# Performance work log

Hardware: AMD Instinct MI355X
Metric: run time of the kernel (lower is better)

## Reference

```python
import jax, jax.numpy as jnp
import numpy as np

ND, NT, B = 16384, 16384, 4096
FD, FT, C = 256, 256, 768


def _gat(x_src, x_dst, ei, Ws, Wd, a_s, a_d, b, num_dst, self_loops):
    """PyG GATConv, heads=1: per-edge attention softmax over incoming edges."""
    if self_loops:
        loops = jnp.arange(num_dst, dtype=ei.dtype)
        ei = jnp.concatenate([ei, jnp.stack([loops, loops])], axis=1)
    src, dst = ei[0], ei[1]
    hs = x_src @ Ws                                   # [Ns, C]
    hd = x_dst @ Wd                                   # [Ndst, C]
    e = jax.nn.leaky_relu((hs @ a_s)[src] + (hd @ a_d)[dst], 0.2)   # [E]
    m = jax.ops.segment_max(e, dst, num_segments=num_dst)
    p = jnp.exp(e - m[dst])
    s = jax.ops.segment_sum(p, dst, num_segments=num_dst)
    alpha = p / (s[dst] + 1e-16)
    out = jax.ops.segment_sum(hs[src] * alpha[:, None], dst, num_segments=num_dst)
    return out + b


def _l2norm(x):
    n = jnp.linalg.norm(x, axis=1, keepdims=True)
    return x / jnp.maximum(n, 1e-12)


def setup_inputs() -> dict:
    ks = iter(jax.random.split(jax.random.key(0), 64))
    def nrm(shape, fan_in=None):
        s = 1.0 if fan_in is None else (1.0 / fan_in) ** 0.5
        return jax.random.normal(next(ks), shape, jnp.float32) * s
    inp = {}
    inp["x_drug"] = nrm((ND, FD))
    inp["x_target"] = nrm((NT, FT))
    inp["cell_features"] = nrm((B, 890))
    for et, fs, fd in (("dd", FD, FD), ("dt", FD, FT), ("tt", FT, FT)):
        inp[f"W_src_{et}"] = nrm((fs, C), fs)
        inp[f"W_dst_{et}"] = nrm((fd, C), fd)
        inp[f"a_src_{et}"] = nrm((C,), C)
        inp[f"a_dst_{et}"] = nrm((C,), C)
        inp[f"b_{et}"] = jnp.zeros((C,), jnp.float32)
    for name, fi, fo in (("red1", 890, 2048), ("red2", 2048, 512), ("red3", 512, 2 * C),
                         ("r2a", 4 * C, 2048), ("r2b", 2048, 512), ("r2c", 512, C), ("cls", C, 2)):
        inp[f"{name}_w"] = nrm((fi, fo), fi)
        inp[f"{name}_b"] = jnp.zeros((fo,), jnp.float32)
    inp["drug1_id"] = jax.random.randint(next(ks), (B,), 0, ND)
    inp["drug2_id"] = jax.random.randint(next(ks), (B,), 0, ND)
    inp["ei_dd"] = jax.random.randint(next(ks), (2, 131072), 0, ND)
    inp["ei_dt"] = jnp.stack([jax.random.randint(next(ks), (262144,), 0, ND),
                              jax.random.randint(next(ks), (262144,), 0, NT)])
    inp["ei_tt"] = jax.random.randint(next(ks), (2, 262144), 0, NT)
    return inp


def reference(x_drug, x_target, cell_features,
              W_src_dd, W_dst_dd, a_src_dd, a_dst_dd, b_dd,
              W_src_dt, W_dst_dt, a_src_dt, a_dst_dt, b_dt,
              W_src_tt, W_dst_tt, a_src_tt, a_dst_tt, b_tt,
              red1_w, red1_b, red2_w, red2_b, red3_w, red3_b,
              r2a_w, r2a_b, r2b_w, r2b_b, r2c_w, r2c_b,
              cls_w, cls_b,
              drug1_id, drug2_id, ei_dd, ei_dt, ei_tt):
    # HeteroConv (aggr='sum') followed by per-type ReLU, num_layers=1
    drug = jax.nn.relu(_gat(x_drug, x_drug, ei_dd,
                            W_src_dd, W_dst_dd, a_src_dd, a_dst_dd, b_dd, ND, True))
    target = jax.nn.relu(
        _gat(x_drug, x_target, ei_dt, W_src_dt, W_dst_dt, a_src_dt, a_dst_dt, b_dt, NT, False)
        + _gat(x_target, x_target, ei_tt, W_src_tt, W_dst_tt, a_src_tt, a_dst_tt, b_tt, NT, True))
    del target  # with num_layers=1 the target embeddings never feed the output (faithful)
    d1 = drug[drug1_id]
    d2 = drug[drug2_id]
    cell = _l2norm(cell_features)
    cell = jax.nn.relu(cell @ red1_w + red1_b)
    cell = jax.nn.relu(cell @ red2_w + red2_b)
    cell = jax.nn.relu(cell @ red3_w + red3_b)          # [B, 2*C]
    hidden = _l2norm(jnp.concatenate([d1, d2, cell], axis=1))  # [B, 4*C]
    hidden = jax.nn.relu(hidden @ r2a_w + r2a_b)
    hidden = jax.nn.relu(hidden @ r2b_w + r2b_b)
    hidden = jax.nn.relu(hidden @ r2c_w + r2c_b)
    return hidden @ cls_w + cls_b                       # [B, 2]
```

## Files before the change

kernel.cpp:

```cpp
#include <hip/hip_runtime.h>
#include <cstdint>

#define ND 16384
#define BATCH 4096
#define CDIM 768
#define E_DD 131072
#define FD 256

typedef unsigned short u16;
typedef u16 u16x4 __attribute__((ext_vector_type(4)));
typedef u16 u16x8 __attribute__((ext_vector_type(8)));
typedef short s16x8 __attribute__((ext_vector_type(8)));
typedef float f32x4 __attribute__((ext_vector_type(4)));

__device__ __forceinline__ u16 f2bf(float x) {
  union { float f; uint32_t u; } v; v.f = x;
  uint32_t r = v.u + 0x7fffu + ((v.u >> 16) & 1u);
  return (u16)(r >> 16);
}
__device__ __forceinline__ float bf2f(u16 h) {
  union { float f; uint32_t u; } v; v.u = ((uint32_t)h) << 16;
  return v.f;
}
__device__ __forceinline__ uint32_t split2p(float x) {
  u16 h = f2bf(x);
  u16 l = f2bf(x - bf2f(h));
  return ((uint32_t)h << 16) | l;
}

#define KP 40

template <int KS, int OUT_BF16, int RELU, int BIAS, int ASPLIT, int ALO, int BLO>
__device__ __forceinline__ void gemm_core(
    int bx, int by, int bz,
    const float* __restrict__ Af,
    const u16* __restrict__ Ahi, const u16* __restrict__ Alo,
    const u16* __restrict__ Bhi, const u16* __restrict__ Blo,
    const float* __restrict__ bias,
    float* __restrict__ Cf, u16* __restrict__ Chi,
    int M, int N, int K, u16* AsB, u16* BsB) {
  constexpr int MT = 4, NT = 4;
  constexpr int BM = 128, BN = 128;
  constexpr int ASEG = BM / 64;
  constexpr int BSEG = BN / 64;

  const int t = threadIdx.x;
  const int bm0 = bx * BM, bn0 = by * BN;
  const int wid = t >> 6, lane = t & 63;
  const int quad = lane >> 4, l16 = lane & 15;
  const int wm0 = (wid >> 1) * (MT * 16);
  const int wn0 = (wid & 1) * (NT * 16);

  const int chunk = K / KS;
  const int kbeg = (KS > 1) ? bz * chunk : 0;
  const int kend = kbeg + chunk;

  auto As = [&](int a, int r, int k) -> u16& { return AsB[(a * BM + r) * KP + k]; };
  auto Bs = [&](int a, int r, int k) -> u16& { return BsB[(a * BN + r) * KP + k]; };

  f32x4 acc[MT][NT];
#pragma unroll
  for (int i = 0; i < MT; ++i)
#pragma unroll
    for (int j = 0; j < NT; ++j) acc[i][j] = (f32x4){0.f, 0.f, 0.f, 0.f};

  u16x8 pAh[ASEG], pAl[ASEG], pBh[BSEG], pBl[BSEG];

  auto loadA = [&](int c, int kk) {
    int s = t + 256 * c, row = s >> 2, kq = (s & 3) * 8;
    size_t off = (size_t)(bm0 + row) * K + kk + kq;
    if (ASPLIT) {
      f32x4 v0 = *(const f32x4*)(Af + off);
      f32x4 v1 = *(const f32x4*)(Af + off + 4);
      u16x8 h, l;
#pragma unroll
      for (int e = 0; e < 4; ++e) {
        uint32_t p = split2p(v0[e]);
        h[e] = (u16)(p >> 16); l[e] = (u16)(p & 0xffffu);
        uint32_t q = split2p(v1[e]);
        h[e + 4] = (u16)(q >> 16); l[e + 4] = (u16)(q & 0xffffu);
      }
      pAh[c] = h; pAl[c] = l;
    } else {
      pAh[c] = *(const u16x8*)(Ahi + off);
      if (ALO) pAl[c] = *(const u16x8*)(Alo + off);
    }
  };
  auto loadB = [&](int c, int kk) {
    int s = t + 256 * c, row = s >> 2, kq = (s & 3) * 8;
    size_t off = (size_t)(bn0 + row) * K + kk + kq;
    pBh[c] = *(const u16x8*)(Bhi + off);
    if (BLO) pBl[c] = *(const u16x8*)(Blo + off);
  };

#pragma unroll
  for (int c = 0; c < ASEG; ++c) loadA(c, kbeg);
#pragma unroll
  for (int c = 0; c < BSEG; ++c) loadB(c, kbeg);

  for (int k0 = kbeg;;) {
    __syncthreads();
#pragma unroll
    for (int c = 0; c < ASEG; ++c) {
      int s = t + 256 * c, row = s >> 2, kq = (s & 3) * 8;
      *(u16x8*)&As(0, row, kq) = pAh[c];
      if (ALO) *(u16x8*)&As(1, row, kq) = pAl[c];
    }
#pragma unroll
    for (int c = 0; c < BSEG; ++c) {
      int s = t + 256 * c, row = s >> 2, kq = (s & 3) * 8;
      *(u16x8*)&Bs(0, row, kq) = pBh[c];
      if (BLO) *(u16x8*)&Bs(1, row, kq) = pBl[c];
    }
    __syncthreads();

    int kn = k0 + 32;
    if (kn < kend) {
#pragma unroll
      for (int c = 0; c < ASEG; ++c) loadA(c, kn);
#pragma unroll
      for (int c = 0; c < BSEG; ++c) loadB(c, kn);
    }

    s16x8 ah[MT], al[MT], bh[NT], bl[NT];
#pragma unroll
    for (int mi = 0; mi < MT; ++mi) {
      ah[mi] = *(const s16x8*)&As(0, wm0 + mi * 16 + l16, quad * 8);
      if (ALO) al[mi] = *(const s16x8*)&As(1, wm0 + mi * 16 + l16, quad * 8);
    }
#pragma unroll
    for (int ni = 0; ni < NT; ++ni) {
      bh[ni] = *(const s16x8*)&Bs(0, wn0 + ni * 16 + l16, quad * 8);
      if (BLO) bl[ni] = *(const s16x8*)&Bs(1, wn0 + ni * 16 + l16, quad * 8);
    }
#pragma unroll
    for (int mi = 0; mi < MT; ++mi)
#pragma unroll
      for (int ni = 0; ni < NT; ++ni) {
        acc[mi][ni] = __builtin_amdgcn_mfma_f32_16x16x32_bf16(
            ah[mi], bh[ni], acc[mi][ni], 0, 0, 0);
        if (BLO)
          acc[mi][ni] = __builtin_amdgcn_mfma_f32_16x16x32_bf16(
              ah[mi], bl[ni], acc[mi][ni], 0, 0, 0);
        if (ALO)
          acc[mi][ni] = __builtin_amdgcn_mfma_f32_16x16x32_bf16(
              al[mi], bh[ni], acc[mi][ni], 0, 0, 0);
      }
    k0 = kn;
    if (k0 >= kend) break;
  }

  float* Cp = (KS > 1) ? Cf + (size_t)bz * M * N : Cf;
#pragma unroll
  for (int mi = 0; mi < MT; ++mi) {
#pragma unroll
    for (int ni = 0; ni < NT; ++ni) {
      int row = bm0 + wm0 + mi * 16 + quad * 4;
      int col = bn0 + wn0 + ni * 16 + l16;
      float bv = BIAS ? bias[col] : 0.f;
#pragma unroll
      for (int r = 0; r < 4; ++r) {
        float v = acc[mi][ni][r] + bv;
        if (RELU) v = fmaxf(v, 0.f);
        size_t o = (size_t)(row + r) * N + col;
        if (OUT_BF16) Chi[o] = f2bf(v);
        else Cp[o] = v;
      }
    }
  }
}

template <int KS, int OUT_BF16, int RELU, int BIAS, int ASPLIT, int ALO, int BLO>
__global__ __launch_bounds__(256) void mfma_gemm(
    const float* __restrict__ Af,
    const u16* __restrict__ Ahi, const u16* __restrict__ Alo,
    const u16* __restrict__ Bhi, const u16* __restrict__ Blo,
    const float* __restrict__ bias,
    float* __restrict__ Cf, u16* __restrict__ Chi,
    int M, int N, int K) {
  __shared__ __align__(16) u16 AsB[(ALO ? 2 : 1) * 128 * KP];
  __shared__ __align__(16) u16 BsB[(BLO ? 2 : 1) * 128 * KP];
  gemm_core<KS, OUT_BF16, RELU, BIAS, ASPLIT, ALO, BLO>(
      blockIdx.x, blockIdx.y, (KS > 1) ? (int)blockIdx.z : 0,
      Af, Ahi, Alo, Bhi, Blo, bias, Cf, Chi, M, N, K, AsB, BsB);
}

__global__ __launch_bounds__(256) void dual_gemm_red1_hs(
    const u16* __restrict__ cn, const u16* __restrict__ r1T,
    const float* __restrict__ red1_b, u16* __restrict__ c1,
    const float* __restrict__ xd, const u16* __restrict__ wsrcT,
    u16* __restrict__ hs) {
  __shared__ __align__(16) u16 AsB[2 * 128 * KP];
  __shared__ __align__(16) u16 BsB[128 * KP];
  int b = blockIdx.x;
  if (b < 512) {
    gemm_core<1, 1, 1, 1, 0, 0, 0>(b & 31, b >> 5, 0, nullptr, cn, nullptr,
                                   r1T, nullptr, red1_b, nullptr, c1,
                                   BATCH, 2048, 896, AsB, BsB);
  } else {
    int b2 = b - 512;
    gemm_core<1, 1, 0, 0, 1, 1, 0>(b2 & 127, b2 >> 7, 0, xd, nullptr, nullptr,
                                   wsrcT, nullptr, nullptr, nullptr, hs,
                                   ND, CDIM, FD, AsB, BsB);
  }
}

template <int KS>
__global__ void reduce_split_ks(const float* __restrict__ P,
                                const float* __restrict__ bias,
                                u16* __restrict__ Chi, int M, int N) {
  int i = blockIdx.x * 256 + threadIdx.x;
  int total = (M * N) >> 2;
  if (i >= total) return;
  f32x4 s = ((const f32x4*)P)[i];
#pragma unroll
  for (int z = 1; z < KS; ++z) s += ((const f32x4*)P)[(size_t)z * total + i];
  int col = (i * 4) % N;
  f32x4 bv = *(const f32x4*)(bias + col);
  u16x4 h;
#pragma unroll
  for (int e = 0; e < 4; ++e) h[e] = f2bf(fmaxf(s[e] + bv[e], 0.f));
  *(u16x4*)&Chi[i * 4] = h;
}

__global__ void reduce_cls(const float* __restrict__ P,
                           const float* __restrict__ bias,
                           const float* __restrict__ clsw,
                           const float* __restrict__ clsb,
                           float* __restrict__ out) {
  int row = blockIdx.x * 4 + (threadIdx.x >> 6);
  int lane = threadIdx.x & 63;
  const f32x4* p0 = (const f32x4*)(P + (size_t)row * CDIM);
  const f32x4* p1 = (const f32x4*)(P + (size_t)BATCH * CDIM + (size_t)row * CDIM);
  float s0 = 0.f, s1 = 0.f;
#pragma unroll
  for (int i = 0; i < 3; ++i) {
    int c4 = lane + 64 * i;
    f32x4 a = p0[c4] + p1[c4];
    f32x4 bv = *(const f32x4*)(bias + c4 * 4);
#pragma unroll
    for (int e = 0; e < 4; ++e) {
      float h = fmaxf(a[e] + bv[e], 0.f);
      int c = c4 * 4 + e;
      s0 = fmaf(h, clsw[c * 2 + 0], s0);
      s1 = fmaf(h, clsw[c * 2 + 1], s1);
    }
  }
#pragma unroll
  for (int m = 32; m; m >>= 1) {
    s0 += __shfl_xor(s0, m);
    s1 += __shfl_xor(s1, m);
  }
  if (lane == 0) {
    out[row * 2 + 0] = s0 + clsb[0];
    out[row * 2 + 1] = s1 + clsb[1];
  }
}

struct TDesc {
  const float* W;
  u16* Th;
  int K, N, Kpad, start;
};
struct TPack { TDesc d[7]; };

__global__ void multi_transpose(TPack p) {
  __shared__ float tile[32][33];
  int b = blockIdx.x;
  int mi = 0;
#pragma unroll
  for (int i = 1; i < 7; ++i)
    if (b >= p.d[i].start) mi = i;
  TDesc dd = p.d[mi];
  int rel = b - dd.start;
  int tilesX = dd.Kpad / 32;
  int k0 = (rel % tilesX) * 32, n0 = (rel / tilesX) * 32;
  int tx = threadIdx.x, ty = threadIdx.y;
#pragma unroll
  for (int i = 0; i < 4; ++i) {
    int k = k0 + ty + 8 * i, n = n0 + tx;
    tile[ty + 8 * i][tx] = (k < dd.K && n < dd.N) ? dd.W[(size_t)k * dd.N + n] : 0.f;
  }
  __syncthreads();
#pragma unroll
  for (int i = 0; i < 4; ++i) {
    int n = n0 + ty + 8 * i, k = k0 + tx;
    if (n < dd.N) dd.Th[(size_t)n * dd.Kpad + k] = f2bf(tile[tx][ty + 8 * i]);
  }
}

__global__ void wvec_kernel(const float* __restrict__ Wsrc,
                            const float* __restrict__ Wdst,
                            const float* __restrict__ a_s,
                            const float* __restrict__ a_d,
                            float* __restrict__ wsv, float* __restrict__ wdv) {
  int k = blockIdx.x;
  int t = threadIdx.x;
  __shared__ float rs[256], rd[256];
  float s = 0.f, d = 0.f;
  for (int c = t; c < CDIM; c += 256) {
    s += Wsrc[(size_t)k * CDIM + c] * a_s[c];
    d += Wdst[(size_t)k * CDIM + c] * a_d[c];
  }
  rs[t] = s; rd[t] = d;
  __syncthreads();
  for (int st = 128; st; st >>= 1) {
    if (t < st) { rs[t] += rs[t + st]; rd[t] += rd[t + st]; }
    __syncthreads();
  }
  if (t == 0) { wsv[k] = rs[0]; wdv[k] = rd[0]; }
}

__global__ void esed_kernel(const float* __restrict__ x,
                            const float* __restrict__ wsv,
                            const float* __restrict__ wdv,
                            float* __restrict__ es, float* __restrict__ ed) {
  int i = blockIdx.x * 256 + threadIdx.x;
  int lane = threadIdx.x & 63;
  int row = i >> 6;
  int c4 = lane * 4;
  f32x4 v = ((const f32x4*)x)[i];
  f32x4 ws = *(const f32x4*)(wsv + c4);
  f32x4 wd = *(const f32x4*)(wdv + c4);
  float a = v[0] * ws[0] + v[1] * ws[1] + v[2] * ws[2] + v[3] * ws[3];
  float b = v[0] * wd[0] + v[1] * wd[1] + v[2] * wd[2] + v[3] * wd[3];
#pragma unroll
  for (int m = 32; m; m >>= 1) {
    a += __shfl_xor(a, m);
    b += __shfl_xor(b, m);
  }
  if (lane == 0) { es[row] = a; ed[row] = b; }
}

__global__ void init_csr(int* counts, int* mask, int* cnt) {
  int i = blockIdx.x * 256 + threadIdx.x;
  if (i < ND) { counts[i] = 1; mask[i] = 0; }
  if (i == 0) *cnt = 0;
}
__global__ void mark_kernel(const int* __restrict__ d1, const int* __restrict__ d2,
                            int* mask) {
  int i = blockIdx.x * 256 + threadIdx.x;
  if (i < BATCH) {
    mask[d1[i]] = 1;
    mask[d2[i]] = 1;
  }
}
__global__ void compact_kernel(const int* __restrict__ mask, int* cnt, int* list) {
  int i = blockIdx.x * 256 + threadIdx.x;
  if (i < ND && mask[i]) {
    int pos = atomicAdd(cnt, 1);
    list[pos] = i;
  }
}

__global__ void count_edges(const int* __restrict__ dst, int* counts) {
  int e = blockIdx.x * 256 + threadIdx.x;
  if (e < E_DD) atomicAdd(&counts[dst[e]], 1);
}
__global__ void scan_kernel(const int* __restrict__ counts, int* __restrict__ offsets,
                            int* __restrict__ cursor, int* __restrict__ slots) {
  __shared__ int part[512];
  int t = threadIdx.x;
  int base = t * 32;
  int s = 0;
  for (int i = 0; i < 32; ++i) s += counts[base + i];
  part[t] = s;
  __syncthreads();
  if (t == 0) {
    int run = 0;
    for (int i = 0; i < 512; ++i) { int tmp = part[i]; part[i] = run; run += tmp; }
    offsets[ND] = run;
  }
  __syncthreads();
  int run = part[t];
  for (int i = 0; i < 32; ++i) {
    int d = base + i;
    offsets[d] = run;
    slots[run] = d;
    cursor[d] = run + 1;
    run += counts[d];
  }
}
__global__ void scatter_edges(const int* __restrict__ src, const int* __restrict__ dst,
                              int* cursor, int* slots) {
  int e = blockIdx.x * 256 + threadIdx.x;
  if (e < E_DD) {
    int pos = atomicAdd(&cursor[dst[e]], 1);
    slots[pos] = src[e];
  }
}

__global__ __launch_bounds__(256) void gat_aggregate(
    const u16* __restrict__ hs, const float* __restrict__ es,
    const float* __restrict__ ed, const int* __restrict__ offsets,
    const int* __restrict__ slots, const float* __restrict__ bias,
    const int* __restrict__ list, const int* __restrict__ cnt,
    u16* __restrict__ out) {
  int idx = blockIdx.x * 4 + (threadIdx.x >> 6);
  if (idx >= *cnt) return;
  int d = list[idx];
  int lane = threadIdx.x & 63;
  int beg = offsets[d], end = offsets[d + 1];
  float edv = ed[d];
  float mx = -1e30f;
  for (int j = beg + lane; j < end; j += 64) {
    float e = es[slots[j]] + edv;
    e = e >= 0.f ? e : 0.2f * e;
    mx = fmaxf(mx, e);
  }
#pragma unroll
  for (int m = 32; m; m >>= 1) mx = fmaxf(mx, __shfl_xor(mx, m));
  float sm = 0.f;
  for (int j = beg + lane; j < end; j += 64) {
    float e = es[slots[j]] + edv;
    e = e >= 0.f ? e : 0.2f * e;
    sm += expf(e - mx);
  }
#pragma unroll
  for (int m = 32; m; m >>= 1) sm += __shfl_xor(sm, m);
  float inv = 1.f / (sm + 1e-16f);
  int c8 = lane * 8;
  int c4 = 512 + lane * 4;
  float a8[8] = {};
  float a4[4] = {};
  for (int j = beg; j < end; ++j) {
    int srcn = slots[j];
    float e = es[srcn] + edv;
    e = e >= 0.f ? e : 0.2f * e;
    float alpha = expf(e - mx) * inv;
    const u16* hrow = hs + (size_t)srcn * CDIM;
    u16x8 r8 = *(const u16x8*)(hrow + c8);
    u16x4 r4 = *(const u16x4*)(hrow + c4);
#pragma unroll
    for (int e2 = 0; e2 < 8; ++e2) a8[e2] = fmaf(alpha, bf2f(r8[e2]), a8[e2]);
#pragma unroll
    for (int e2 = 0; e2 < 4; ++e2) a4[e2] = fmaf(alpha, bf2f(r4[e2]), a4[e2]);
  }
  u16* orow = out + (size_t)d * CDIM;
  u16x8 o8;
  u16x4 o4;
#pragma unroll
  for (int e2 = 0; e2 < 8; ++e2) o8[e2] = f2bf(fmaxf(a8[e2] + bias[c8 + e2], 0.f));
#pragma unroll
  for (int e2 = 0; e2 < 4; ++e2) o4[e2] = f2bf(fmaxf(a4[e2] + bias[c4 + e2], 0.f));
  *(u16x8*)(orow + c8) = o8;
  *(u16x4*)(orow + c4) = o4;
}

__global__ void l2norm_bf16(const float* __restrict__ in, u16* __restrict__ hi,
                            int L, int Lp) {
  int row = blockIdx.x;
  int t = threadIdx.x;
  __shared__ float red[256];
  const float* irow = in + (size_t)row * L;
  float s = 0.f;
  for (int c = t; c < L; c += 256) { float v = irow[c]; s += v * v; }
  red[t] = s;
  __syncthreads();
  for (int st = 128; st; st >>= 1) {
    if (t < st) red[t] += red[t + st];
    __syncthreads();
  }
  float inv = 1.f / fmaxf(sqrtf(red[0]), 1e-12f);
  for (int c = t; c < Lp; c += 256) {
    float v = (c < L) ? irow[c] * inv : 0.f;
    hi[(size_t)row * Lp + c] = f2bf(v);
  }
}

__global__ __launch_bounds__(256) void hidden_build_bf16(
    const u16* __restrict__ drug, const u16* __restrict__ c3,
    const int* __restrict__ d1, const int* __restrict__ d2,
    u16* __restrict__ hhi) {
  int row = blockIdx.x;
  int t = threadIdx.x;
  const u16* s1 = drug + (size_t)d1[row] * CDIM;
  const u16* s2 = drug + (size_t)d2[row] * CDIM;
  const u16* s3 = c3 + (size_t)row * (2 * CDIM);
  float vals[12];
// ... 53 lines not shown
  const int* dd_src = ei_dd;
  const int* dd_dst = ei_dd + E_DD;

  char* w = (char*)d_ws;
  size_t off = 0;
  auto alloc = [&](size_t bytes) -> char* {
    char* p = w + off;
    off = (off + bytes + 255) & ~(size_t)255;
    return p;
  };
  u16* hs   = (u16*)alloc((size_t)ND * CDIM * 2);
  u16* drug = (u16*)alloc((size_t)ND * CDIM * 2);
  u16* c3   = (u16*)alloc((size_t)BATCH * 2 * CDIM * 2);
  float* P  = (float*)alloc((size_t)4 * BATCH * 512 * 4);
  u16* hid_hi = hs;
  u16* cn_hi = (u16*)alloc((size_t)BATCH * 896 * 2);
  u16* c1_hi = (u16*)alloc((size_t)BATCH * 2048 * 2);
  u16* c2_hi = (u16*)alloc((size_t)BATCH * 512 * 2);
  u16* wsrcT_hi = (u16*)alloc((size_t)CDIM * FD * 2);
  u16* r1T_hi = (u16*)alloc((size_t)2048 * 896 * 2);
  u16* r2T_hi = (u16*)alloc((size_t)512 * 2048 * 2);
  u16* r3T_hi = (u16*)alloc((size_t)1536 * 512 * 2);
  u16* raT_hi = (u16*)alloc((size_t)2048 * 3072 * 2);
  u16* rbT_hi = (u16*)alloc((size_t)512 * 2048 * 2);
  u16* rcT_hi = (u16*)alloc((size_t)768 * 512 * 2);
  float* es  = (float*)alloc((size_t)ND * 4);
  float* ed  = (float*)alloc((size_t)ND * 4);
  float* wsv = (float*)alloc(FD * 4);
  float* wdv = (float*)alloc(FD * 4);
  int* counts  = (int*)alloc((size_t)ND * 4);
  int* offsets = (int*)alloc((size_t)(ND + 1) * 4);
  int* cursor  = (int*)alloc((size_t)ND * 4);
  int* slots   = (int*)alloc((size_t)(E_DD + ND) * 4);
  int* mask    = (int*)alloc((size_t)ND * 4);
  int* list    = (int*)alloc((size_t)ND * 4);
  int* cnt     = (int*)alloc(256);
  (void)ws_size; (void)n_in; (void)in_sizes; (void)out_size;

  TPack tp;
  tp.d[0] = {W_src_dd, wsrcT_hi, 256, 768, 256, 0};
  tp.d[1] = {red1_w, r1T_hi, 890, 2048, 896, 192};
  tp.d[2] = {red2_w, r2T_hi, 2048, 512, 2048, 1984};
  tp.d[3] = {red3_w, r3T_hi, 512, 1536, 512, 3008};
  tp.d[4] = {r2a_w, raT_hi, 3072, 2048, 3072, 3776};
  tp.d[5] = {r2b_w, rbT_hi, 2048, 512, 2048, 9920};
  tp.d[6] = {r2c_w, rcT_hi, 512, 768, 512, 10944};
  multi_transpose<<<11328, dim3(32, 8), 0, stream>>>(tp);

  wvec_kernel<<<FD, 256, 0, stream>>>(W_src_dd, W_dst_dd, a_src_dd, a_dst_dd, wsv, wdv);
  esed_kernel<<<ND * FD / 1024, 256, 0, stream>>>(x_drug, wsv, wdv, es, ed);
  init_csr<<<ND / 256, 256, 0, stream>>>(counts, mask, cnt);
  mark_kernel<<<BATCH / 256, 256, 0, stream>>>(drug1_id, drug2_id, mask);
  compact_kernel<<<ND / 256, 256, 0, stream>>>(mask, cnt, list);
  l2norm_bf16<<<BATCH, 256, 0, stream>>>(cellf, cn_hi, 890, 896);

  dual_gemm_red1_hs<<<1280, 256, 0, stream>>>(cn_hi, r1T_hi, red1_b, c1_hi,
                                              x_drug, wsrcT_hi, hs);

  mfma_gemm<4, 0, 0, 0, 0, 0, 0><<<dim3(BATCH / 128, 512 / 128, 4), 256, 0, stream>>>(
      nullptr, c1_hi, nullptr, r2T_hi, nullptr, nullptr, P, nullptr, BATCH, 512, 2048);
  reduce_split_ks<4><<<BATCH * 512 / 1024, 256, 0, stream>>>(P, red2_b, c2_hi, BATCH, 512);
  mfma_gemm<1, 1, 1, 1, 0, 0, 0><<<dim3(BATCH / 128, 1536 / 128), 256, 0, stream>>>(
      nullptr, c2_hi, nullptr, r3T_hi, nullptr, red3_b, nullptr, c3, BATCH, 1536, 512);

  count_edges<<<E_DD / 256, 256, 0, stream>>>(dd_dst, counts);
  scan_kernel<<<1, 512, 0, stream>>>(counts, offsets, cursor, slots);
  scatter_edges<<<E_DD / 256, 256, 0, stream>>>(dd_src, dd_dst, cursor, slots);
  gat_aggregate<<<ND / 4, 256, 0, stream>>>(hs, es, ed, offsets, slots, b_dd, list, cnt, drug);

  hidden_build_bf16<<<BATCH, 256, 0, stream>>>(drug, c3, drug1_id, drug2_id, hid_hi);

  mfma_gemm<1, 1, 1, 1, 0, 0, 0><<<dim3(BATCH / 128, 2048 / 128), 256, 0, stream>>>(
      nullptr, hid_hi, nullptr, raT_hi, nullptr, r2a_b, nullptr, c1_hi, BATCH, 2048, 3072);
  mfma_gemm<4, 0, 0, 0, 0, 0, 0><<<dim3(BATCH / 128, 512 / 128, 4), 256, 0, stream>>>(
      nullptr, c1_hi, nullptr, rbT_hi, nullptr, nullptr, P, nullptr, BATCH, 512, 2048);
  reduce_split_ks<4><<<BATCH * 512 / 1024, 256, 0, stream>>>(P, r2b_b, c2_hi, BATCH, 512);
  mfma_gemm<2, 0, 0, 0, 0, 0, 0><<<dim3(BATCH / 128, CDIM / 128, 2), 256, 0, stream>>>(
      nullptr, c2_hi, nullptr, rcT_hi, nullptr, nullptr, P, nullptr, BATCH, CDIM, 512);
  reduce_cls<<<BATCH / 4, 256, 0, stream>>>(P, r2c_b, cls_w, cls_b, out);
}
```

Baseline: 479.6 us.

## Co-schedule red2 split-K GEMM with GAT aggregation; narrow N tile for r2a GEMM

Merges the red2 split-K GEMM and the GAT aggregation into one launch, with block index deciding which work each block does, so the two independent stages run concurrently and fill the GPU. The edge CSR build is moved earlier so its results are ready for the fused launch. The gemm core gains an NT template parameter, and the r2a GEMM uses 128x64 tiles to produce more blocks. The trade-offs are more kernel code and the larger shared-memory footprint of the fused kernel, which may limit occupancy for the GAT blocks. Narrower tiles also reuse loaded data less.

```diff
diff --git a/kernel.cpp b/kernel.cpp
--- a/kernel.cpp
+++ b/kernel.cpp
@@ -30,7 +30,8 @@
 
 #define KP 40
 
-template <int KS, int OUT_BF16, int RELU, int BIAS, int ASPLIT, int ALO, int BLO>
+template <int KS, int OUT_BF16, int RELU, int BIAS, int ASPLIT, int ALO, int BLO,
+          int NT>
 __device__ __forceinline__ void gemm_core(
     int bx, int by, int bz,
     const float* __restrict__ Af,
@@ -39,8 +40,8 @@
     const float* __restrict__ bias,
     float* __restrict__ Cf, u16* __restrict__ Chi,
     int M, int N, int K, u16* AsB, u16* BsB) {
-  constexpr int MT = 4, NT = 4;
-  constexpr int BM = 128, BN = 128;
+  constexpr int MT = 4;
+  constexpr int BM = 128, BN = NT * 32;
   constexpr int ASEG = BM / 64;
   constexpr int BSEG = BN / 64;
 
@@ -88,9 +89,11 @@
   };
   auto loadB = [&](int c, int kk) {
     int s = t + 256 * c, row = s >> 2, kq = (s & 3) * 8;
-    size_t off = (size_t)(bn0 + row) * K + kk + kq;
-    pBh[c] = *(const u16x8*)(Bhi + off);
-    if (BLO) pBl[c] = *(const u16x8*)(Blo + off);
+    if (row < BN) {
+      size_t off = (size_t)(bn0 + row) * K + kk + kq;
+      pBh[c] = *(const u16x8*)(Bhi + off);
+      if (BLO) pBl[c] = *(const u16x8*)(Blo + off);
+    }
   };
 
 #pragma unroll
@@ -109,8 +112,10 @@
 #pragma unroll
     for (int c = 0; c < BSEG; ++c) {
       int s = t + 256 * c, row = s >> 2, kq = (s & 3) * 8;
-      *(u16x8*)&Bs(0, row, kq) = pBh[c];
-      if (BLO) *(u16x8*)&Bs(1, row, kq) = pBl[c];
+      if (row < BN) {
+        *(u16x8*)&Bs(0, row, kq) = pBh[c];
+        if (BLO) *(u16x8*)&Bs(1, row, kq) = pBl[c];
+      }
     }
     __syncthreads();
 
@@ -170,7 +175,8 @@
   }
 }
 
-template <int KS, int OUT_BF16, int RELU, int BIAS, int ASPLIT, int ALO, int BLO>
+template <int KS, int OUT_BF16, int RELU, int BIAS, int ASPLIT, int ALO, int BLO,
+          int NT = 4>
 __global__ __launch_bounds__(256) void mfma_gemm(
     const float* __restrict__ Af,
     const u16* __restrict__ Ahi, const u16* __restrict__ Alo,
@@ -179,224 +185,18 @@
     float* __restrict__ Cf, u16* __restrict__ Chi,
     int M, int N, int K) {
   __shared__ __align__(16) u16 AsB[(ALO ? 2 : 1) * 128 * KP];
-  __shared__ __align__(16) u16 BsB[(BLO ? 2 : 1) * 128 * KP];
-  gemm_core<KS, OUT_BF16, RELU, BIAS, ASPLIT, ALO, BLO>(
+  __shared__ __align__(16) u16 BsB[(BLO ? 2 : 1) * (NT * 32) * KP];
+  gemm_core<KS, OUT_BF16, RELU, BIAS, ASPLIT, ALO, BLO, NT>(
       blockIdx.x, blockIdx.y, (KS > 1) ? (int)blockIdx.z : 0,
       Af, Ahi, Alo, Bhi, Blo, bias, Cf, Chi, M, N, K, AsB, BsB);
 }
 
-__global__ __launch_bounds__(256) void dual_gemm_red1_hs(
-    const u16* __restrict__ cn, const u16* __restrict__ r1T,
-    const float* __restrict__ red1_b, u16* __restrict__ c1,
-    const float* __restrict__ xd, const u16* __restrict__ wsrcT,
-    u16* __restrict__ hs) {
-  __shared__ __align__(16) u16 AsB[2 * 128 * KP];
-  __shared__ __align__(16) u16 BsB[128 * KP];
-  int b = blockIdx.x;
-  if (b < 512) {
-    gemm_core<1, 1, 1, 1, 0, 0, 0>(b & 31, b >> 5, 0, nullptr, cn, nullptr,
-                                   r1T, nullptr, red1_b, nullptr, c1,
-                                   BATCH, 2048, 896, AsB, BsB);
-  } else {
-    int b2 = b - 512;
-    gemm_core<1, 1, 0, 0, 1, 1, 0>(b2 & 127, b2 >> 7, 0, xd, nullptr, nullptr,
-                                   wsrcT, nullptr, nullptr, nullptr, hs,
-                                   ND, CDIM, FD, AsB, BsB);
-  }
-}
-
-template <int KS>
-__global__ void reduce_split_ks(const float* __restrict__ P,
-                                const float* __restrict__ bias,
-                                u16* __restrict__ Chi, int M, int N) {
-  int i = blockIdx.x * 256 + threadIdx.x;
-  int total = (M * N) >> 2;
-  if (i >= total) return;
-  f32x4 s = ((const f32x4*)P)[i];
-#pragma unroll
-  for (int z = 1; z < KS; ++z) s += ((const f32x4*)P)[(size_t)z * total + i];
-  int col = (i * 4) % N;
-  f32x4 bv = *(const f32x4*)(bias + col);
-  u16x4 h;
-#pragma unroll
-  for (int e = 0; e < 4; ++e) h[e] = f2bf(fmaxf(s[e] + bv[e], 0.f));
-  *(u16x4*)&Chi[i * 4] = h;
-}
-
-__global__ void reduce_cls(const float* __restrict__ P,
-                           const float* __restrict__ bias,
-                           const float* __restrict__ clsw,
-                           const float* __restrict__ clsb,
-                           float* __restrict__ out) {
-  int row = blockIdx.x * 4 + (threadIdx.x >> 6);
-  int lane = threadIdx.x & 63;
-  const f32x4* p0 = (const f32x4*)(P + (size_t)row * CDIM);
-  const f32x4* p1 = (const f32x4*)(P + (size_t)BATCH * CDIM + (size_t)row * CDIM);
-  float s0 = 0.f, s1 = 0.f;
-#pragma unroll
-  for (int i = 0; i < 3; ++i) {
-    int c4 = lane + 64 * i;
-    f32x4 a = p0[c4] + p1[c4];
-    f32x4 bv = *(const f32x4*)(bias + c4 * 4);
-#pragma unroll
-    for (int e = 0; e < 4; ++e) {
-      float h = fmaxf(a[e] + bv[e], 0.f);
-      int c = c4 * 4 + e;
-      s0 = fmaf(h, clsw[c * 2 + 0], s0);
-      s1 = fmaf(h, clsw[c * 2 + 1], s1);
-    }
-  }
-#pragma unroll
-  for (int m = 32; m; m >>= 1) {
-    s0 += __shfl_xor(s0, m);
-    s1 += __shfl_xor(s1, m);
-  }
-  if (lane == 0) {
-    out[row * 2 + 0] = s0 + clsb[0];
-    out[row * 2 + 1] = s1 + clsb[1];
-  }
-}
-
-struct TDesc {
-  const float* W;
-  u16* Th;
-  int K, N, Kpad, start;
-};
-struct TPack { TDesc d[7]; };
-
-__global__ void multi_transpose(TPack p) {
-  __shared__ float tile[32][33];
-  int b = blockIdx.x;
-  int mi = 0;
-#pragma unroll
-  for (int i = 1; i < 7; ++i)
-    if (b >= p.d[i].start) mi = i;
-  TDesc dd = p.d[mi];
-  int rel = b - dd.start;
-  int tilesX = dd.Kpad / 32;
-  int k0 = (rel % tilesX) * 32, n0 = (rel / tilesX) * 32;
-  int tx = threadIdx.x, ty = threadIdx.y;
-#pragma unroll
-  for (int i = 0; i < 4; ++i) {
-    int k = k0 + ty + 8 * i, n = n0 + tx;
-    tile[ty + 8 * i][tx] = (k < dd.K && n < dd.N) ? dd.W[(size_t)k * dd.N + n] : 0.f;
-  }
-  __syncthreads();
-#pragma unroll
-  for (int i = 0; i < 4; ++i) {
-    int n = n0 + ty + 8 * i, k = k0 + tx;
-    if (n < dd.N) dd.Th[(size_t)n * dd.Kpad + k] = f2bf(tile[tx][ty + 8 * i]);
-  }
-}
-
-__global__ void wvec_kernel(const float* __restrict__ Wsrc,
-                            const float* __restrict__ Wdst,
-                            const float* __restrict__ a_s,
-                            const float* __restrict__ a_d,
-                            float* __restrict__ wsv, float* __restrict__ wdv) {
-  int k = blockIdx.x;
-  int t = threadIdx.x;
-  __shared__ float rs[256], rd[256];
-  float s = 0.f, d = 0.f;
-  for (int c = t; c < CDIM; c += 256) {
-    s += Wsrc[(size_t)k * CDIM + c] * a_s[c];
-    d += Wdst[(size_t)k * CDIM + c] * a_d[c];
-  }
-  rs[t] = s; rd[t] = d;
-  __syncthreads();
-  for (int st = 128; st; st >>= 1) {
-    if (t < st) { rs[t] += rs[t + st]; rd[t] += rd[t + st]; }
-    __syncthreads();
-  }
-  if (t == 0) { wsv[k] = rs[0]; wdv[k] = rd[0]; }
-}
-
-__global__ void esed_kernel(const float* __restrict__ x,
-                            const float* __restrict__ wsv,
-                            const float* __restrict__ wdv,
-                            float* __restrict__ es, float* __restrict__ ed) {
-  int i = blockIdx.x * 256 + threadIdx.x;
-  int lane = threadIdx.x & 63;
-  int row = i >> 6;
-  int c4 = lane * 4;
-  f32x4 v = ((const f32x4*)x)[i];
-  f32x4 ws = *(const f32x4*)(wsv + c4);
-  f32x4 wd = *(const f32x4*)(wdv + c4);
-  float a = v[0] * ws[0] + v[1] * ws[1] + v[2] * ws[2] + v[3] * ws[3];
-  float b = v[0] * wd[0] + v[1] * wd[1] + v[2] * wd[2] + v[3] * wd[3];
-#pragma unroll
-  for (int m = 32; m; m >>= 1) {
-    a += __shfl_xor(a, m);
-    b += __shfl_xor(b, m);
-  }
-  if (lane == 0) { es[row] = a; ed[row] = b; }
-}
-
-__global__ void init_csr(int* counts, int* mask, int* cnt) {
-  int i = blockIdx.x * 256 + threadIdx.x;
-  if (i < ND) { counts[i] = 1; mask[i] = 0; }
-  if (i == 0) *cnt = 0;
-}
-__global__ void mark_kernel(const int* __restrict__ d1, const int* __restrict__ d2,
-                            int* mask) {
-  int i = blockIdx.x * 256 + threadIdx.x;
-  if (i < BATCH) {
-    mask[d1[i]] = 1;
-    mask[d2[i]] = 1;
-  }
-}
-__global__ void compact_kernel(const int* __restrict__ mask, int* cnt, int* list) {
-  int i = blockIdx.x * 256 + threadIdx.x;
-  if (i < ND && mask[i]) {
-    int pos = atomicAdd(cnt, 1);
-    list[pos] = i;
-  }
-}
-
-__global__ void count_edges(const int* __restrict__ dst, int* counts) {
-  int e = blockIdx.x * 256 + threadIdx.x;
-  if (e < E_DD) atomicAdd(&counts[dst[e]], 1);
-}
-__global__ void scan_kernel(const int* __restrict__ counts, int* __restrict__ offsets,
-                            int* __restrict__ cursor, int* __restrict__ slots) {
-  __shared__ int part[512];
-  int t = threadIdx.x;
-  int base = t * 32;
-  int s = 0;
-  for (int i = 0; i < 32; ++i) s += counts[base + i];
-  part[t] = s;
-  __syncthreads();
-  if (t == 0) {
-    int run = 0;
-    for (int i = 0; i < 512; ++i) { int tmp = part[i]; part[i] = run; run += tmp; }
-    offsets[ND] = run;
-  }
-  __syncthreads();
-  int run = part[t];
-  for (int i = 0; i < 32; ++i) {
-    int d = base + i;
-    offsets[d] = run;
-    slots[run] = d;
-    cursor[d] = run + 1;
-    run += counts[d];
-  }
-}
-__global__ void scatter_edges(const int* __restrict__ src, const int* __restrict__ dst,
-                              int* cursor, int* slots) {
-  int e = blockIdx.x * 256 + threadIdx.x;
-  if (e < E_DD) {
-    int pos = atomicAdd(&cursor[dst[e]], 1);
-    slots[pos] = src[e];
-  }
-}
-
-__global__ __launch_bounds__(256) void gat_aggregate(
-    const u16* __restrict__ hs, const float* __restrict__ es,
+__device__ __forceinline__ void gat_body(
+    int idx, const u16* __restrict__ hs, const float* __restrict__ es,
     const float* __restrict__ ed, const int* __restrict__ offsets,
     const int* __restrict__ slots, const float* __restrict__ bias,
     const int* __restrict__ list, const int* __restrict__ cnt,
     u16* __restrict__ out) {
-  int idx = blockIdx.x * 4 + (threadIdx.x >> 6);
   if (idx >= *cnt) return;
   int d = list[idx];
   int lane = threadIdx.x & 63;
@@ -445,6 +245,232 @@
   for (int e2 = 0; e2 < 4; ++e2) o4[e2] = f2bf(fmaxf(a4[e2] + bias[c4 + e2], 0.f));
   *(u16x8*)(orow + c8) = o8;
   *(u16x4*)(orow + c4) = o4;
+}
+
+__global__ __launch_bounds__(256) void dual_gemm_red1_hs(
+    const u16* __restrict__ cn, const u16* __restrict__ r1T,
+    const float* __restrict__ red1_b, u16* __restrict__ c1,
+    const float* __restrict__ xd, const u16* __restrict__ wsrcT,
+    u16* __restrict__ hs) {
+  __shared__ __align__(16) u16 AsB[2 * 128 * KP];
+  __shared__ __align__(16) u16 BsB[128 * KP];
+  int b = blockIdx.x;
+  if (b < 512) {
+    gemm_core<1, 1, 1, 1, 0, 0, 0, 4>(b & 31, b >> 5, 0, nullptr, cn, nullptr,
+                                      r1T, nullptr, red1_b, nullptr, c1,
+                                      BATCH, 2048, 896, AsB, BsB);
+  } else {
+    int b2 = b - 512;
+    gemm_core<1, 1, 0, 0, 1, 1, 0, 4>(b2 & 127, b2 >> 7, 0, xd, nullptr, nullptr,
+                                      wsrcT, nullptr, nullptr, nullptr, hs,
+                                      ND, CDIM, FD, AsB, BsB);
+  }
+}
+
+__global__ __launch_bounds__(256) void dual_red2_gat(
+    const u16* __restrict__ c1, const u16* __restrict__ r2T,
+    float* __restrict__ P,
+    const u16* __restrict__ hs, const float* __restrict__ es,
+    const float* __restrict__ ed, const int* __restrict__ offsets,
+    const int* __restrict__ slots, const float* __restrict__ bias,
+    const int* __restrict__ list, const int* __restrict__ cnt,
+    u16* __restrict__ drug) {
+  __shared__ __align__(16) u16 AsB[128 * KP];
+  __shared__ __align__(16) u16 BsB[128 * KP];
+  int b = blockIdx.x;
+  if (b < 512) {
+    gemm_core<4, 0, 0, 0, 0, 0, 0, 4>(b & 31, (b >> 5) & 3, b >> 7, nullptr,
+                                      c1, nullptr, r2T, nullptr, nullptr, P,
+                                      nullptr, BATCH, 512, 2048, AsB, BsB);
+  } else {
+    int idx = (b - 512) * 4 + (threadIdx.x >> 6);
+    gat_body(idx, hs, es, ed, offsets, slots, bias, list, cnt, drug);
+  }
+}
+
+template <int KS>
+__global__ void reduce_split_ks(const float* __restrict__ P,
+                                const float* __restrict__ bias,
+                                u16* __restrict__ Chi, int M, int N) {
+  int i = blockIdx.x * 256 + threadIdx.x;
+  int total = (M * N) >> 2;
+  if (i >= total) return;
+  f32x4 s = ((const f32x4*)P)[i];
+#pragma unroll
+  for (int z = 1; z < KS; ++z) s += ((const f32x4*)P)[(size_t)z * total + i];
+  int col = (i * 4) % N;
+  f32x4 bv = *(const f32x4*)(bias + col);
+  u16x4 h;
+#pragma unroll
+  for (int e = 0; e < 4; ++e) h[e] = f2bf(fmaxf(s[e] + bv[e], 0.f));
+  *(u16x4*)&Chi[i * 4] = h;
+}
+
+__global__ void reduce_cls(const float* __restrict__ P,
+                           const float* __restrict__ bias,
+                           const float* __restrict__ clsw,
+                           const float* __restrict__ clsb,
+                           float* __restrict__ out) {
+  int row = blockIdx.x * 4 + (threadIdx.x >> 6);
+  int lane = threadIdx.x & 63;
+  const f32x4* p0 = (const f32x4*)(P + (size_t)row * CDIM);
+  const f32x4* p1 = (const f32x4*)(P + (size_t)BATCH * CDIM + (size_t)row * CDIM);
+  float s0 = 0.f, s1 = 0.f;
+#pragma unroll
+  for (int i = 0; i < 3; ++i) {
+    int c4 = lane + 64 * i;
+    f32x4 a = p0[c4] + p1[c4];
+    f32x4 bv = *(const f32x4*)(bias + c4 * 4);
+#pragma unroll
+    for (int e = 0; e < 4; ++e) {
+      float h = fmaxf(a[e] + bv[e], 0.f);
+      int c = c4 * 4 + e;
+      s0 = fmaf(h, clsw[c * 2 + 0], s0);
+      s1 = fmaf(h, clsw[c * 2 + 1], s1);
+    }
+  }
+#pragma unroll
+  for (int m = 32; m; m >>= 1) {
+    s0 += __shfl_xor(s0, m);
+    s1 += __shfl_xor(s1, m);
+  }
+  if (lane == 0) {
+    out[row * 2 + 0] = s0 + clsb[0];
+    out[row * 2 + 1] = s1 + clsb[1];
+  }
+}
+
+struct TDesc {
+  const float* W;
+  u16* Th;
+  int K, N, Kpad, start;
+};
+struct TPack { TDesc d[7]; };
+
+__global__ void multi_transpose(TPack p) {
+  __shared__ float tile[32][33];
+  int b = blockIdx.x;
+  int mi = 0;
+#pragma unroll
+  for (int i = 1; i < 7; ++i)
+    if (b >= p.d[i].start) mi = i;
+  TDesc dd = p.d[mi];
+  int rel = b - dd.start;
+  int tilesX = dd.Kpad / 32;
+  int k0 = (rel % tilesX) * 32, n0 = (rel / tilesX) * 32;
+  int tx = threadIdx.x, ty = threadIdx.y;
+#pragma unroll
+  for (int i = 0; i < 4; ++i) {
+    int k = k0 + ty + 8 * i, n = n0 + tx;
+    tile[ty + 8 * i][tx] = (k < dd.K && n < dd.N) ? dd.W[(size_t)k * dd.N + n] : 0.f;
+  }
+  __syncthreads();
+#pragma unroll
+  for (int i = 0; i < 4; ++i) {
+    int n = n0 + ty + 8 * i, k = k0 + tx;
+    if (n < dd.N) dd.Th[(size_t)n * dd.Kpad + k] = f2bf(tile[tx][ty + 8 * i]);
+  }
+}
+
+__global__ void wvec_kernel(const float* __restrict__ Wsrc,
+                            const float* __restrict__ Wdst,
+                            const float* __restrict__ a_s,
+                            const float* __restrict__ a_d,
+                            float* __restrict__ wsv, float* __restrict__ wdv) {
+  int k = blockIdx.x;
+  int t = threadIdx.x;
+  __shared__ float rs[256], rd[256];
+  float s = 0.f, d = 0.f;
+  for (int c = t; c < CDIM; c += 256) {
+    s += Wsrc[(size_t)k * CDIM + c] * a_s[c];
+    d += Wdst[(size_t)k * CDIM + c] * a_d[c];
+  }
+  rs[t] = s; rd[t] = d;
+  __syncthreads();
+  for (int st = 128; st; st >>= 1) {
+    if (t < st) { rs[t] += rs[t + st]; rd[t] += rd[t + st]; }
+    __syncthreads();
+  }
+  if (t == 0) { wsv[k] = rs[0]; wdv[k] = rd[0]; }
+}
+
+__global__ void esed_kernel(const float* __restrict__ x,
+                            const float* __restrict__ wsv,
+                            const float* __restrict__ wdv,
+                            float* __restrict__ es, float* __restrict__ ed) {
+  int i = blockIdx.x * 256 + threadIdx.x;
+  int lane = threadIdx.x & 63;
+  int row = i >> 6;
+  int c4 = lane * 4;
+  f32x4 v = ((const f32x4*)x)[i];
+  f32x4 ws = *(const f32x4*)(wsv + c4);
+  f32x4 wd = *(const f32x4*)(wdv + c4);
+  float a = v[0] * ws[0] + v[1] * ws[1] + v[2] * ws[2] + v[3] * ws[3];
+  float b = v[0] * wd[0] + v[1] * wd[1] + v[2] * wd[2] + v[3] * wd[3];
+#pragma unroll
+  for (int m = 32; m; m >>= 1) {
+    a += __shfl_xor(a, m);
+    b += __shfl_xor(b, m);
+  }
+  if (lane == 0) { es[row] = a; ed[row] = b; }
+}
+
+__global__ void init_csr(int* counts, int* mask, int* cnt) {
+  int i = blockIdx.x * 256 + threadIdx.x;
+  if (i < ND) { counts[i] = 1; mask[i] = 0; }
+  if (i == 0) *cnt = 0;
+}
+__global__ void mark_kernel(const int* __restrict__ d1, const int* __restrict__ d2,
+                            int* mask) {
+  int i = blockIdx.x * 256 + threadIdx.x;
+  if (i < BATCH) {
+    mask[d1[i]] = 1;
+    mask[d2[i]] = 1;
+  }
+}
+__global__ void compact_kernel(const int* __restrict__ mask, int* cnt, int* list) {
+  int i = blockIdx.x * 256 + threadIdx.x;
+  if (i < ND && mask[i]) {
+    int pos = atomicAdd(cnt, 1);
+    list[pos] = i;
+  }
+}
+
+__global__ void count_edges(const int* __restrict__ dst, int* counts) {
+  int e = blockIdx.x * 256 + threadIdx.x;
+  if (e < E_DD) atomicAdd(&counts[dst[e]], 1);
+}
+__global__ void scan_kernel(const int* __restrict__ counts, int* __restrict__ offsets,
+                            int* __restrict__ cursor, int* __restrict__ slots) {
+  __shared__ int part[512];
+  int t = threadIdx.x;
+  int base = t * 32;
+  int s = 0;
+  for (int i = 0; i < 32; ++i) s += counts[base + i];
+  part[t] = s;
+  __syncthreads();
+  if (t == 0) {
+    int run = 0;
+    for (int i = 0; i < 512; ++i) { int tmp = part[i]; part[i] = run; run += tmp; }
+    offsets[ND] = run;
+  }
+  __syncthreads();
+  int run = part[t];
+  for (int i = 0; i < 32; ++i) {
+    int d = base + i;
+    offsets[d] = run;
+    slots[run] = d;
+    cursor[d] = run + 1;
+    run += counts[d];
+  }
+}
+__global__ void scatter_edges(const int* __restrict__ src, const int* __restrict__ dst,
+                              int* cursor, int* slots) {
+  int e = blockIdx.x * 256 + threadIdx.x;
+  if (e < E_DD) {
+    int pos = atomicAdd(&cursor[dst[e]], 1);
+    slots[pos] = src[e];
+  }
 }
 
 __global__ void l2norm_bf16(const float* __restrict__ in, u16* __restrict__ hi,
@@ -584,30 +610,28 @@
   init_csr<<<ND / 256, 256, 0, stream>>>(counts, mask, cnt);
   mark_kernel<<<BATCH / 256, 256, 0, stream>>>(drug1_id, drug2_id, mask);
   compact_kernel<<<ND / 256, 256, 0, stream>>>(mask, cnt, list);
-  l2norm_bf16<<<BATCH, 256, 0, stream>>>(cellf, cn_hi, 890, 896);
-
-  dual_gemm_red1_hs<<<1280, 256, 0, stream>>>(cn_hi, r1T_hi, red1_b, c1_hi,
-                                              x_drug, wsrcT_hi, hs);
-
-  mfma_gemm<4, 0, 0, 0, 0, 0, 0><<<dim3(BATCH / 128, 512 / 128, 4), 256, 0, stream>>>(
-      nullptr, c1_hi, nullptr, r2T_hi, nullptr, nullptr, P, nullptr, BATCH, 512, 2048);
-  reduce_split_ks<4><<<BATCH * 512 / 1024, 256, 0, stream>>>(P, red2_b, c2_hi, BATCH, 512);
-  mfma_gemm<1, 1, 1, 1, 0, 0, 0><<<dim3(BATCH / 128, 1536 / 128), 256, 0, stream>>>(
-      nullptr, c2_hi, nullptr, r3T_hi, nullptr, red3_b, nullptr, c3, BATCH, 1536, 512);
-
   count_edges<<<E_DD / 256, 256, 0, stream>>>(dd_dst, counts);
   scan_kernel<<<1, 512, 0, stream>>>(counts, offsets, cursor, slots);
   scatter_edges<<<E_DD / 256, 256, 0, stream>>>(dd_src, dd_dst, cursor, slots);
-  gat_aggregate<<<ND / 4, 256, 0, stream>>>(hs, es, ed, offsets, slots, b_dd, list, cnt, drug);
+  l2norm_bf16<<<BATCH, 256, 0, stream>>>(cellf, cn_hi, 890, 896);
+
+  dual_gemm_red1_hs<<<1280, 256, 0, stream>>>(cn_hi, r1T_hi, red1_b, c1_hi,
+                                              x_drug, wsrcT_hi, hs);
+
+  dual_red2_gat<<<512 + ND / 4, 256, 0, stream>>>(
+      c1_hi, r2T_hi, P, hs, es, ed, offsets, slots, b_dd, list, cnt, drug);
+  reduce_split_ks<4><<<BATCH * 512 / 1024, 256, 0, stream>>>(P, red2_b, c2_hi, BATCH, 512);
+  mfma_gemm<1, 1, 1, 1, 0, 0, 0, 4><<<dim3(BATCH / 128, 1536 / 128), 256, 0, stream>>>(
+      nullptr, c2_hi, nullptr, r3T_hi, nullptr, red3_b, nullptr, c3, BATCH, 1536, 512);
 
   hidden_build_bf16<<<BATCH, 256, 0, stream>>>(drug, c3, drug1_id, drug2_id, hid_hi);
 
-  mfma_gemm<1, 1, 1, 1, 0, 0, 0><<<dim3(BATCH / 128, 2048 / 128), 256, 0, stream>>>(
+  mfma_gemm<1, 1, 1, 1, 0, 0, 0, 2><<<dim3(BATCH / 128, 2048 / 64), 256, 0, stream>>>(
       nullptr, hid_hi, nullptr, raT_hi, nullptr, r2a_b, nullptr, c1_hi, BATCH, 2048, 3072);
-  mfma_gemm<4, 0, 0, 0, 0, 0, 0><<<dim3(BATCH / 128, 512 / 128, 4), 256, 0, stream>>>(
+  mfma_gemm<4, 0, 0, 0, 0, 0, 0, 4><<<dim3(BATCH / 128, 512 / 128, 4), 256, 0, stream>>>(
       nullptr, c1_hi, nullptr, rbT_hi, nullptr, nullptr, P, nullptr, BATCH, 512, 2048);
   reduce_split_ks<4><<<BATCH * 512 / 1024, 256, 0, stream>>>(P, r2b_b, c2_hi, BATCH, 512);
-  mfma_gemm<2, 0, 0, 0, 0, 0, 0><<<dim3(BATCH / 128, CDIM / 128, 2), 256, 0, stream>>>(
+  mfma_gemm<2, 0, 0, 0, 0, 0, 0, 4><<<dim3(BATCH / 128, CDIM / 128, 2), 256, 0, stream>>>(
       nullptr, c2_hi, nullptr, rcT_hi, nullptr, nullptr, P, nullptr, BATCH, CDIM, 512);
   reduce_cls<<<BATCH / 4, 256, 0, stream>>>(P, r2c_b, cls_w, cls_b, out);
 }
```

Result: slower. 501.1 us (+4.5%).

## Fuse GAT aggregation into red2 split-K GEMM launch and drop mask compaction

Applied to the files above, without the earlier changes.

Removes the mask, mark and compact kernels. The GAT aggregation now runs directly per batch index (d1 and d2), so duplicate drug rows may be computed redundantly with identical writes. The counts initialisation is folded into the esed kernel, and CSR construction moves earlier in the stream. GAT aggregation is co-scheduled inside the same launch as the red2 split-K GEMM blocks, so the memory-latency-bound gather overlaps compute-bound MFMA work and several launches disappear. The cost is some duplicated gather work for repeated drug ids.

```diff
diff --git a/kernel.cpp b/kernel.cpp
--- a/kernel.cpp
+++ b/kernel.cpp
@@ -183,6 +183,62 @@
   gemm_core<KS, OUT_BF16, RELU, BIAS, ASPLIT, ALO, BLO>(
       blockIdx.x, blockIdx.y, (KS > 1) ? (int)blockIdx.z : 0,
       Af, Ahi, Alo, Bhi, Blo, bias, Cf, Chi, M, N, K, AsB, BsB);
+}
+
+__device__ __forceinline__ void gat_body(
+    int idx, const u16* __restrict__ hs, const float* __restrict__ es,
+    const float* __restrict__ ed, const int* __restrict__ offsets,
+    const int* __restrict__ slots, const float* __restrict__ bias,
+    const int* __restrict__ d1, const int* __restrict__ d2,
+    u16* __restrict__ out) {
+  if (idx >= 2 * BATCH) return;
+  int d = (idx < BATCH) ? d1[idx] : d2[idx - BATCH];
+  int lane = threadIdx.x & 63;
+  int beg = offsets[d], end = offsets[d + 1];
+  float edv = ed[d];
+  float mx = -1e30f;
+  for (int j = beg + lane; j < end; j += 64) {
+    float e = es[slots[j]] + edv;
+    e = e >= 0.f ? e : 0.2f * e;
+    mx = fmaxf(mx, e);
+  }
+#pragma unroll
+  for (int m = 32; m; m >>= 1) mx = fmaxf(mx, __shfl_xor(mx, m));
+  float sm = 0.f;
+  for (int j = beg + lane; j < end; j += 64) {
+    float e = es[slots[j]] + edv;
+    e = e >= 0.f ? e : 0.2f * e;
+    sm += expf(e - mx);
+  }
+#pragma unroll
+  for (int m = 32; m; m >>= 1) sm += __shfl_xor(sm, m);
+  float inv = 1.f / (sm + 1e-16f);
+  int c8 = lane * 8;
+  int c4 = 512 + lane * 4;
+  float a8[8] = {};
+  float a4[4] = {};
+  for (int j = beg; j < end; ++j) {
+    int srcn = slots[j];
+    float e = es[srcn] + edv;
+    e = e >= 0.f ? e : 0.2f * e;
+    float alpha = expf(e - mx) * inv;
+    const u16* hrow = hs + (size_t)srcn * CDIM;
+    u16x8 r8 = *(const u16x8*)(hrow + c8);
+    u16x4 r4 = *(const u16x4*)(hrow + c4);
+#pragma unroll
+    for (int e2 = 0; e2 < 8; ++e2) a8[e2] = fmaf(alpha, bf2f(r8[e2]), a8[e2]);
+#pragma unroll
+    for (int e2 = 0; e2 < 4; ++e2) a4[e2] = fmaf(alpha, bf2f(r4[e2]), a4[e2]);
+  }
+  u16* orow = out + (size_t)d * CDIM;
+  u16x8 o8;
+  u16x4 o4;
+#pragma unroll
+  for (int e2 = 0; e2 < 8; ++e2) o8[e2] = f2bf(fmaxf(a8[e2] + bias[c8 + e2], 0.f));
+#pragma unroll
+  for (int e2 = 0; e2 < 4; ++e2) o4[e2] = f2bf(fmaxf(a4[e2] + bias[c4 + e2], 0.f));
+  *(u16x8*)(orow + c8) = o8;
+  *(u16x4*)(orow + c4) = o4;
 }
 
 __global__ __launch_bounds__(256) void dual_gemm_red1_hs(
@@ -205,6 +261,27 @@
   }
 }
 
+__global__ __launch_bounds__(256) void dual_red2_gat(
+    const u16* __restrict__ c1, const u16* __restrict__ r2T,
+    float* __restrict__ P,
+    const u16* __restrict__ hs, const float* __restrict__ es,
+    const float* __restrict__ ed, const int* __restrict__ offsets,
+    const int* __restrict__ slots, const float* __restrict__ bias,
+    const int* __restrict__ d1, const int* __restrict__ d2,
+    u16* __restrict__ drug) {
+  __shared__ __align__(16) u16 AsB[128 * KP];
+  __shared__ __align__(16) u16 BsB[128 * KP];
+  int b = blockIdx.x;
+  if (b < 512) {
+    gemm_core<4, 0, 0, 0, 0, 0, 0>(b & 31, (b >> 5) & 3, b >> 7, nullptr,
+                                   c1, nullptr, r2T, nullptr, nullptr, P,
+                                   nullptr, BATCH, 512, 2048, AsB, BsB);
+  } else {
+    int idx = (b - 512) * 4 + (threadIdx.x >> 6);
+    gat_body(idx, hs, es, ed, offsets, slots, bias, d1, d2, drug);
+  }
+}
+
 template <int KS>
 __global__ void reduce_split_ks(const float* __restrict__ P,
                                 const float* __restrict__ bias,
@@ -314,7 +391,9 @@
 __global__ void esed_kernel(const float* __restrict__ x,
                             const float* __restrict__ wsv,
                             const float* __restrict__ wdv,
-                            float* __restrict__ es, float* __restrict__ ed) {
+                            float* __restrict__ es, float* __restrict__ ed,
+                            int* __restrict__ counts) {
+  if (blockIdx.x < 64) counts[blockIdx.x * 256 + threadIdx.x] = 1;
   int i = blockIdx.x * 256 + threadIdx.x;
   int lane = threadIdx.x & 63;
   int row = i >> 6;
@@ -330,27 +409,6 @@
     b += __shfl_xor(b, m);
   }
   if (lane == 0) { es[row] = a; ed[row] = b; }
-}
-
-__global__ void init_csr(int* counts, int* mask, int* cnt) {
-  int i = blockIdx.x * 256 + threadIdx.x;
-  if (i < ND) { counts[i] = 1; mask[i] = 0; }
-  if (i == 0) *cnt = 0;
-}
-__global__ void mark_kernel(const int* __restrict__ d1, const int* __restrict__ d2,
-                            int* mask) {
-  int i = blockIdx.x * 256 + threadIdx.x;
-  if (i < BATCH) {
-    mask[d1[i]] = 1;
-    mask[d2[i]] = 1;
-  }
-}
-__global__ void compact_kernel(const int* __restrict__ mask, int* cnt, int* list) {
-  int i = blockIdx.x * 256 + threadIdx.x;
-  if (i < ND && mask[i]) {
-    int pos = atomicAdd(cnt, 1);
-    list[pos] = i;
-  }
 }
 
 __global__ void count_edges(const int* __restrict__ dst, int* counts) {
@@ -388,63 +446,6 @@
     int pos = atomicAdd(&cursor[dst[e]], 1);
     slots[pos] = src[e];
   }
-}
-
-__global__ __launch_bounds__(256) void gat_aggregate(
-    const u16* __restrict__ hs, const float* __restrict__ es,
-    const float* __restrict__ ed, const int* __restrict__ offsets,
-    const int* __restrict__ slots, const float* __restrict__ bias,
-    const int* __restrict__ list, const int* __restrict__ cnt,
-    u16* __restrict__ out) {
-  int idx = blockIdx.x * 4 + (threadIdx.x >> 6);
-  if (idx >= *cnt) return;
-  int d = list[idx];
-  int lane = threadIdx.x & 63;
-  int beg = offsets[d], end = offsets[d + 1];
-  float edv = ed[d];
-  float mx = -1e30f;
-  for (int j = beg + lane; j < end; j += 64) {
-    float e = es[slots[j]] + edv;
-    e = e >= 0.f ? e : 0.2f * e;
-    mx = fmaxf(mx, e);
-  }
-#pragma unroll
-  for (int m = 32; m; m >>= 1) mx = fmaxf(mx, __shfl_xor(mx, m));
-  float sm = 0.f;
-  for (int j = beg + lane; j < end; j += 64) {
-    float e = es[slots[j]] + edv;
-    e = e >= 0.f ? e : 0.2f * e;
-    sm += expf(e - mx);
-  }
-#pragma unroll
-  for (int m = 32; m; m >>= 1) sm += __shfl_xor(sm, m);
-  float inv = 1.f / (sm + 1e-16f);
-  int c8 = lane * 8;
-  int c4 = 512 + lane * 4;
-  float a8[8] = {};
-  float a4[4] = {};
-  for (int j = beg; j < end; ++j) {
-    int srcn = slots[j];
-    float e = es[srcn] + edv;
-    e = e >= 0.f ? e : 0.2f * e;
-    float alpha = expf(e - mx) * inv;
-    const u16* hrow = hs + (size_t)srcn * CDIM;
-    u16x8 r8 = *(const u16x8*)(hrow + c8);
-    u16x4 r4 = *(const u16x4*)(hrow + c4);
-#pragma unroll
-    for (int e2 = 0; e2 < 8; ++e2) a8[e2] = fmaf(alpha, bf2f(r8[e2]), a8[e2]);
-#pragma unroll
-    for (int e2 = 0; e2 < 4; ++e2) a4[e2] = fmaf(alpha, bf2f(r4[e2]), a4[e2]);
-  }
-  u16* orow = out + (size_t)d * CDIM;
-  u16x8 o8;
-  u16x4 o4;
-#pragma unroll
-  for (int e2 = 0; e2 < 8; ++e2) o8[e2] = f2bf(fmaxf(a8[e2] + bias[c8 + e2], 0.f));
-#pragma unroll
-  for (int e2 = 0; e2 < 4; ++e2) o4[e2] = f2bf(fmaxf(a4[e2] + bias[c4 + e2], 0.f));
-  *(u16x8*)(orow + c8) = o8;
-  *(u16x4*)(orow + c4) = o4;
 }
 
 __global__ void l2norm_bf16(const float* __restrict__ in, u16* __restrict__ hi,
@@ -564,9 +565,6 @@
   int* offsets = (int*)alloc((size_t)(ND + 1) * 4);
   int* cursor  = (int*)alloc((size_t)ND * 4);
   int* slots   = (int*)alloc((size_t)(E_DD + ND) * 4);
-  int* mask    = (int*)alloc((size_t)ND * 4);
-  int* list    = (int*)alloc((size_t)ND * 4);
-  int* cnt     = (int*)alloc(256);
   (void)ws_size; (void)n_in; (void)in_sizes; (void)out_size;
 
   TPack tp;
@@ -580,25 +578,20 @@
   multi_transpose<<<11328, dim3(32, 8), 0, stream>>>(tp);
 
   wvec_kernel<<<FD, 256, 0, stream>>>(W_src_dd, W_dst_dd, a_src_dd, a_dst_dd, wsv, wdv);
-  esed_kernel<<<ND * FD / 1024, 256, 0, stream>>>(x_drug, wsv, wdv, es, ed);
-  init_csr<<<ND / 256, 256, 0, stream>>>(counts, mask, cnt);
-  mark_kernel<<<BATCH / 256, 256, 0, stream>>>(drug1_id, drug2_id, mask);
-  compact_kernel<<<ND / 256, 256, 0, stream>>>(mask, cnt, list);
+  esed_kernel<<<ND * FD / 1024, 256, 0, stream>>>(x_drug, wsv, wdv, es, ed, counts);
+  count_edges<<<E_DD / 256, 256, 0, stream>>>(dd_dst, counts);
+  scan_kernel<<<1, 512, 0, stream>>>(counts, offsets, cursor, slots);
+  scatter_edges<<<E_DD / 256, 256, 0, stream>>>(dd_src, dd_dst, cursor, slots);
   l2norm_bf16<<<BATCH, 256, 0, stream>>>(cellf, cn_hi, 890, 896);
 
   dual_gemm_red1_hs<<<1280, 256, 0, stream>>>(cn_hi, r1T_hi, red1_b, c1_hi,
                                               x_drug, wsrcT_hi, hs);
 
-  mfma_gemm<4, 0, 0, 0, 0, 0, 0><<<dim3(BATCH / 128, 512 / 128, 4), 256, 0, stream>>>(
-      nullptr, c1_hi, nullptr, r2T_hi, nullptr, nullptr, P, nullptr, BATCH, 512, 2048);
+  dual_red2_gat<<<512 + 2 * BATCH / 4, 256, 0, stream>>>(
+      c1_hi, r2T_hi, P, hs, es, ed, offsets, slots, b_dd, drug1_id, drug2_id, drug);
   reduce_split_ks<4><<<BATCH * 512 / 1024, 256, 0, stream>>>(P, red2_b, c2_hi, BATCH, 512);
   mfma_gemm<1, 1, 1, 1, 0, 0, 0><<<dim3(BATCH / 128, 1536 / 128), 256, 0, stream>>>(
       nullptr, c2_hi, nullptr, r3T_hi, nullptr, red3_b, nullptr, c3, BATCH, 1536, 512);
-
-  count_edges<<<E_DD / 256, 256, 0, stream>>>(dd_dst, counts);
-  scan_kernel<<<1, 512, 0, stream>>>(counts, offsets, cursor, slots);
-  scatter_edges<<<E_DD / 256, 256, 0, stream>>>(dd_src, dd_dst, cursor, slots);
-  gat_aggregate<<<ND / 4, 256, 0, stream>>>(hs, es, ed, offsets, slots, b_dd, list, cnt, drug);
 
   hidden_build_bf16<<<BATCH, 256, 0, stream>>>(drug, c3, drug1_id, drug2_id, hid_hi);
 
```

After: 493.9 us. 1.03x slower.
